# Performance work log

Hardware: AMD Instinct MI355X
Metric: run time of the kernel (lower is better)

Reference implementation:

```python
import jax, jax.numpy as jnp
import numpy as np

B, T, N, C, D = 8, 12, 1024, 64, 10

def setup_inputs() -> dict:
    key = jax.random.key(0)
    ks = jax.random.split(key, 7)
    x = jax.random.normal(ks[0], (B, T, N, C), dtype=jnp.float32)
    e1 = jax.random.normal(ks[1], (N, D), dtype=jnp.float32)
    e2 = jax.random.normal(ks[2], (N, D), dtype=jnp.float32)
    # buffer: sym-normalized adjacency after the __init__-time softmax
    A_sym = jax.random.uniform(ks[3], (N, N), dtype=jnp.float32)
    weights_pool = jax.random.normal(ks[4], (N, C, C), dtype=jnp.float32) * 0.02
    bias_pool = jax.random.normal(ks[5], (N, C), dtype=jnp.float32) * 0.02
    alpha = jnp.array([0.9], dtype=jnp.float32)
    beta = jnp.array([0.9], dtype=jnp.float32)
    gamma = jnp.array([0.1], dtype=jnp.float32)
    return {"x": x, "node_embeddings1": e1, "node_embeddings2": e2,
            "A_sym": A_sym, "weights_pool": weights_pool, "bias_pool": bias_pool,
            "alpha": alpha, "beta": beta, "gamma": gamma}


def reference(x, node_embeddings1, node_embeddings2, A_sym, weights_pool,
              bias_pool, alpha, beta, gamma):
    n = node_embeddings1.shape[0]
    # dynamic supports: relu(tanh(E1 E2^T - E2 E1^T)) + I
    s = jnp.tanh(node_embeddings1 @ node_embeddings2.T
                 - node_embeddings2 @ node_embeddings1.T)
    supports = jnp.eye(n, dtype=x.dtype) + jax.nn.relu(s)          # (N,N)

    # static branch: row-softmax of the precomputed sym-norm adjacency
    A = jax.nn.softmax(A_sym, axis=-1)                              # (N,N)
    x_static = jax.nn.relu(jnp.einsum('nm,btmc->btnc', A, x))       # (B,T,N,C)

    # spatial attention branch (note: softmax over the TIME axis, as in source)
    score = jnp.einsum('btnc,btmc->btnm', x, x)                     # (B,T,N,N)
    score = jax.nn.softmax(score, axis=1)
    x_sa = jax.nn.relu(jnp.einsum('btnm,btmc->btnc', score, x))     # (B,T,N,C)

    # adaptive graph conv: per-node weights/bias from supports
    weights = jnp.einsum('nd,dio->nio', supports, weights_pool)     # (N,C,C)
    bias = supports @ bias_pool                                     # (N,C)
    x_g = jnp.einsum('nm,btmc->btnc', supports, x)                  # (B,T,N,C)
    x_gconv = jax.nn.relu(jnp.einsum('btni,nio->btno', x_g, weights) + bias)

    return alpha * x_gconv + beta * x_sa + gamma * x_static
```

## Files before the change

### kernel.cpp

```cpp
#include <hip/hip_runtime.h>
#include <math.h>

#define Bdim 8
#define Tdim 12
#define BT   96
#define Ndim 1024
#define Cdim 64
#define Ddim 10
#define Jdim 6144
#define IOdim 4096

typedef __attribute__((ext_vector_type(4))) float f32x4;
typedef __attribute__((ext_vector_type(8))) short bf16x8;
typedef __attribute__((ext_vector_type(4))) _Float16 f16x4;

__device__ inline short f2bf(float f) {
    union { float f; unsigned u; } v; v.f = f;
    return (short)((v.u + 0x8000u) >> 16);
}
__device__ inline float bf2f(short s) {
    union { float f; unsigned u; } v; v.u = ((unsigned)(unsigned short)s) << 16;
    return v.f;
}
__device__ inline void load_lds16(const void* g, void* l) {
    __builtin_amdgcn_global_load_lds(
        (const __attribute__((address_space(1))) unsigned int*)g,
        (__attribute__((address_space(3))) unsigned int*)l, 16, 0, 0);
}
__device__ inline float fexp(float x) { return __expf(x); }
__device__ inline float frcp(float x) { return __builtin_amdgcn_rcpf(x); }
__device__ inline float flog(float x) { return __logf(x); }

__global__ __launch_bounds__(256) void k_supports(
    const float* __restrict__ e1, const float* __restrict__ e2,
    short* __restrict__ Sbf)
{
    int idx = blockIdx.x * 256 + threadIdx.x;
    int i = idx >> 10, j = idx & 1023;
    float s = 0.f;
#pragma unroll
    for (int d = 0; d < Ddim; ++d)
        s += e1[i * Ddim + d] * e2[j * Ddim + d]
           - e2[i * Ddim + d] * e1[j * Ddim + d];
    float t = 1.f - 2.f * frcp(fexp(2.f * s) + 1.f);
    float v = fmaxf(t, 0.f);
    if (i == j) v += 1.f;
    Sbf[idx] = f2bf(v);
}

__global__ __launch_bounds__(256) void k_softmax_rows(
    const float* __restrict__ In, short* __restrict__ Out)
{
    int row = blockIdx.x;
    const float* r = In + (size_t)row * Ndim;
    short* o = Out + (size_t)row * Ndim;
    __shared__ float red[256];
    int tid = threadIdx.x;
    float vals[4];
    float lmax = -INFINITY;
#pragma unroll
    for (int i = 0; i < 4; ++i) { vals[i] = r[tid + 256 * i]; lmax = fmaxf(lmax, vals[i]); }
    red[tid] = lmax; __syncthreads();
    for (int s = 128; s > 0; s >>= 1) {
        if (tid < s) red[tid] = fmaxf(red[tid], red[tid + s]);
        __syncthreads();
    }
    float m = red[0]; __syncthreads();
    float lsum = 0.f;
#pragma unroll
    for (int i = 0; i < 4; ++i) { vals[i] = fexp(vals[i] - m); lsum += vals[i]; }
    red[tid] = lsum; __syncthreads();
    for (int s = 128; s > 0; s >>= 1) {
        if (tid < s) red[tid] += red[tid + s];
        __syncthreads();
    }
    float inv = frcp(red[0]);
#pragma unroll
    for (int i = 0; i < 4; ++i) o[tid + 256 * i] = f2bf(vals[i] * inv);
}

__global__ __launch_bounds__(256) void k_cvt_x(
    const float* __restrict__ x, short* __restrict__ xbf, short* __restrict__ xT)
{
    __shared__ float Lt[64][65];
    int bt = blockIdx.y, n0 = blockIdx.x * 64;
    const float* src = x + (size_t)bt * 65536 + (size_t)n0 * 64;
    int tid = threadIdx.x;
#pragma unroll
    for (int p = 0; p < 4; ++p) {
        int idx = p * 256 + tid;
        int r = idx >> 4, c4 = idx & 15;
        float4 v = *(const float4*)&src[r * 64 + c4 * 4];
        short4 s4 = make_short4(f2bf(v.x), f2bf(v.y), f2bf(v.z), f2bf(v.w));
        *(short4*)&xbf[(size_t)bt * 65536 + (size_t)(n0 + r) * 64 + c4 * 4] = s4;
        Lt[r][c4 * 4 + 0] = v.x; Lt[r][c4 * 4 + 1] = v.y;
        Lt[r][c4 * 4 + 2] = v.z; Lt[r][c4 * 4 + 3] = v.w;
    }
    __syncthreads();
#pragma unroll
    for (int p = 0; p < 4; ++p) {
        int idx = p * 256 + tid;
        int c = idx >> 4, k4 = idx & 15;
        short4 s4 = make_short4(f2bf(Lt[k4 * 4 + 0][c]), f2bf(Lt[k4 * 4 + 1][c]),
                                f2bf(Lt[k4 * 4 + 2][c]), f2bf(Lt[k4 * 4 + 3][c]));
        *(short4*)&xT[(size_t)bt * 65536 + (size_t)c * 1024 + n0 + k4 * 4] = s4;
    }
}

__global__ __launch_bounds__(256) void k_cvt_wp(
    const float* __restrict__ wp, short* __restrict__ wpT)
{
    __shared__ float Lt[64][65];
    int k0 = blockIdx.y * 64, j0 = blockIdx.x * 64;
    int tid = threadIdx.x;
#pragma unroll
    for (int p = 0; p < 4; ++p) {
        int idx = p * 256 + tid;
        int r = idx >> 4, c4 = idx & 15;
        float4 v = *(const float4*)&wp[(size_t)(k0 + r) * IOdim + j0 + c4 * 4];
        Lt[r][c4 * 4 + 0] = v.x; Lt[r][c4 * 4 + 1] = v.y;
        Lt[r][c4 * 4 + 2] = v.z; Lt[r][c4 * 4 + 3] = v.w;
    }
    __syncthreads();
#pragma unroll
    for (int p = 0; p < 4; ++p) {
        int idx = p * 256 + tid;
        int c = idx >> 4, k4 = idx & 15;
        short4 s4 = make_short4(f2bf(Lt[k4 * 4 + 0][c]), f2bf(Lt[k4 * 4 + 1][c]),
                                f2bf(Lt[k4 * 4 + 2][c]), f2bf(Lt[k4 * 4 + 3][c]));
        *(short4*)&wpT[(size_t)(j0 + c) * 1024 + k0 + k4 * 4] = s4;
    }
}

__global__ __launch_bounds__(256) void k_cvt_bp(
    const float* __restrict__ bp, short* __restrict__ bpT)
{
    __shared__ float Lt[64][65];
    int k0 = blockIdx.x * 64;
    int tid = threadIdx.x;
#pragma unroll
    for (int p = 0; p < 4; ++p) {
        int idx = p * 256 + tid;
        int r = idx >> 4, c4 = idx & 15;
        float4 v = *(const float4*)&bp[(size_t)(k0 + r) * 64 + c4 * 4];
        Lt[r][c4 * 4 + 0] = v.x; Lt[r][c4 * 4 + 1] = v.y;
        Lt[r][c4 * 4 + 2] = v.z; Lt[r][c4 * 4 + 3] = v.w;
    }
    __syncthreads();
#pragma unroll
    for (int p = 0; p < 4; ++p) {
        int idx = p * 256 + tid;
        int c = idx >> 4, k4 = idx & 15;
        short4 s4 = make_short4(f2bf(Lt[k4 * 4 + 0][c]), f2bf(Lt[k4 * 4 + 1][c]),
                                f2bf(Lt[k4 * 4 + 2][c]), f2bf(Lt[k4 * 4 + 3][c]));
        *(short4*)&bpT[(size_t)c * 1024 + k0 + k4 * 4] = s4;
    }
}

template<int MODE>
__global__ __launch_bounds__(256) void k_gemm_bt(
    const short* __restrict__ A, const short* __restrict__ Bm,
    float* __restrict__ Cf, short* __restrict__ Cb,
    const float* __restrict__ gamma_p)
{
    __shared__ short At[128 * 64];
    __shared__ short Bt[128 * 64];
    const int tid = threadIdx.x;
    const int w = tid >> 6, l = tid & 63;
    const int l15 = l & 15, q = l >> 4;
    const int n0 = blockIdx.x * 128, j0 = blockIdx.y * 128;
    const int wr = (w & 1) * 64, wc = (w >> 1) * 64;
    const int lrow = l >> 3, lc8 = l & 7;

    f32x4 acc[4][4];
#pragma unroll
    for (int i = 0; i < 4; ++i)
#pragma unroll
        for (int j = 0; j < 4; ++j) acc[i][j] = (f32x4)0.f;

    for (int k0 = 0; k0 < 1024; k0 += 64) {
        __syncthreads();
#pragma unroll
        for (int p = 0; p < 4; ++p) {
            int r = p * 32 + w * 8 + lrow;
            int sc = lc8 ^ (r & 7);
            load_lds16(A + (size_t)(n0 + r) * 1024 + k0 + sc * 8,
                       &At[(p * 32 + w * 8) * 64]);
            load_lds16(Bm + (size_t)(j0 + r) * 1024 + k0 + sc * 8,
                       &Bt[(p * 32 + w * 8) * 64]);
        }
        __syncthreads();
#pragma unroll
        for (int ks = 0; ks < 2; ++ks) {
            bf16x8 af[4], bf[4];
#pragma unroll
            for (int rt = 0; rt < 4; ++rt) {
                int row = wr + rt * 16 + l15;
                int pos = (ks * 4 + q) ^ (row & 7);
                af[rt] = *(const bf16x8*)&At[row * 64 + pos * 8];
            }
#pragma unroll
            for (int ct = 0; ct < 4; ++ct) {
                int row = wc + ct * 16 + l15;
                int pos = (ks * 4 + q) ^ (row & 7);
                bf[ct] = *(const bf16x8*)&Bt[row * 64 + pos * 8];
            }
#pragma unroll
            for (int rt = 0; rt < 4; ++rt)
#pragma unroll
                for (int ct = 0; ct < 4; ++ct)
                    acc[rt][ct] = __builtin_amdgcn_mfma_f32_16x16x32_bf16(
                        af[rt], bf[ct], acc[rt][ct], 0, 0, 0);
        }
    }

    float gmm = (MODE == 0) ? gamma_p[0] : 0.f;
#pragma unroll
    for (int rt = 0; rt < 4; ++rt) {
        int nr = n0 + wr + rt * 16 + q * 4;
#pragma unroll
        for (int ct = 0; ct < 4; ++ct) {
            int j = j0 + wc + ct * 16 + l15;
#pragma unroll
            for (int r = 0; r < 4; ++r) {
                float v = acc[rt][ct][r];
                int n = nr + r;
                if (MODE == 1) {
                    Cb[(size_t)n * IOdim + j] = f2bf(v);
                } else if (n < 1024) {
                    int bt = j >> 6, c = j & 63;
                    Cf[(size_t)bt * 65536 + (size_t)n * 64 + c] = gmm * fmaxf(v, 0.f);
                } else {
                    Cb[(size_t)(n - 1024) * Jdim + j] = f2bf(v);
                }
            }
        }
    }
}

__global__ __launch_bounds__(256, 4) void k_sa_z(
    const short* __restrict__ xbf, short* __restrict__ Lh)
{
    __shared__ short Xn[64 * 64];
    __shared__ short Xm[64 * 64];

    int id = blockIdx.x;
    int b = id & 7;
    int r = id >> 3;
    int tn = 0, rr = r;
    while (rr >= 16 - tn) { rr -= 16 - tn; ++tn; }
    int tm = tn + rr;
    int tid = threadIdx.x;
    int w = tid >> 6, l = tid & 63;
    int l15 = l & 15, q = l >> 4;
    int lrow = l >> 3, lc8 = l & 7;
    int n0 = tn * 64, m0 = tm * 64;
    int wn = (w & 1) * 32, wm = (w >> 1) * 32;

    const short* Xb = xbf + (size_t)b * Tdim * Ndim * Cdim;
    short* Lb = Lh + ((size_t)b << 20);

    f32x4 M[2][2], Z[2][2];
#pragma unroll
    for (int nh = 0; nh < 2; ++nh)
#pragma unroll
        for (int mh = 0; mh < 2; ++mh) { M[nh][mh] = (f32x4)(-INFINITY); Z[nh][mh] = (f32x4)0.f; }

    for (int t = 0; t < Tdim; ++t) {
        const short* xt = Xb + (size_t)t * (Ndim * Cdim);
        __syncthreads();
#pragma unroll
        for (int p = 0; p < 2; ++p) {
            int rw = p * 32 + w * 8 + lrow;
            int sc = lc8 ^ (rw & 7);
            load_lds16(xt + (size_t)(n0 + rw) * 64 + sc * 8, &Xn[(p * 32 + w * 8) * 64]);
            load_lds16(xt + (size_t)(m0 + rw) * 64 + sc * 8, &Xm[(p * 32 + w * 8) * 64]);
        }
        __syncthreads();

        f32x4 sacc[2][2];
        sacc[0][0] = (f32x4)0.f; sacc[0][1] = (f32x4)0.f;
        sacc[1][0] = (f32x4)0.f; sacc[1][1] = (f32x4)0.f;
#pragma unroll
        for (int ch = 0; ch < 2; ++ch) {
            bf16x8 qb[2], af[2];
#pragma unroll
            for (int nh = 0; nh < 2; ++nh) {
                int row = wn + nh * 16 + l15;
                int pos = (ch * 4 + q) ^ (row & 7);
                qb[nh] = *(const bf16x8*)&Xn[row * 64 + pos * 8];
            }
#pragma unroll
            for (int mh = 0; mh < 2; ++mh) {
                int row = wm + mh * 16 + l15;
                int pos = (ch * 4 + q) ^ (row & 7);
                af[mh] = *(const bf16x8*)&Xm[row * 64 + pos * 8];
            }
#pragma unroll
            for (int nh = 0; nh < 2; ++nh)
#pragma unroll
                for (int mh = 0; mh < 2; ++mh)
                    sacc[nh][mh] = __builtin_amdgcn_mfma_f32_16x16x32_bf16(
                        af[mh], qb[nh], sacc[nh][mh], 0, 0, 0);
        }
#pragma unroll
        for (int nh = 0; nh < 2; ++nh)
#pragma unroll
            for (int mh = 0; mh < 2; ++mh)
#pragma unroll
                for (int i = 0; i < 4; ++i) {
                    float s  = sacc[nh][mh][i];
                    float mo = M[nh][mh][i];
                    float mn = fmaxf(mo, s);
                    Z[nh][mh][i] = Z[nh][mh][i] * fexp(mo - mn) + fexp(s - mn);
                    M[nh][mh][i] = mn;
                }
    }
#pragma unroll
    for (int nh = 0; nh < 2; ++nh)
#pragma unroll
        for (int mh = 0; mh < 2; ++mh) {
            f16x4 ev;
#pragma unroll
            for (int i = 0; i < 4; ++i)
                ev[i] = (_Float16)(M[nh][mh][i] + flog(Z[nh][mh][i]));
            int nn = n0 + wn + nh * 16 + l15;
            int mm = m0 + wm + mh * 16 + q * 4;
            *(f16x4*)&Lb[(size_t)nn * 1024 + mm] = ev;
            if (tn != tm) {
#pragma unroll
                for (int i = 0; i < 4; ++i)
                    Lb[(size_t)(mm + i) * 1024 + nn] = ((short*)&ev)[i];
            }
        }
}

__global__ __launch_bounds__(256, 3) void k_sa_pv(
    const short* __restrict__ xbf, const short* __restrict__ xT,
    const short* __restrict__ Lh, float* __restrict__ Out,
    const float* __restrict__ beta_p)
{
    __shared__ short Xm[2][64 * 64];
    __shared__ short XTl[2][64 * 64];
    __shared__ short Pl[4][16 * 64];

    int id = blockIdx.x;
    int b = id & 7;
    int r = id >> 3;
    int nt = r & 7, t = r >> 3;
    int tid = threadIdx.x;
    int w = tid >> 6, l = tid & 63;
    int l15 = l & 15, q = l >> 4;
    int n0 = nt * 128 + w * 32;

    const short* Xb  = xbf + ((size_t)b * Tdim + t) * (Ndim * Cdim);
    const short* XTb = xT  + ((size_t)b * Tdim + t) * (Ndim * Cdim);
    const short* Lb  = Lh + ((size_t)b << 20);

    int srow = tid >> 2, sc4 = tid & 3;

    bf16x8 qf[2][2];
#pragma unroll
    for (int nh = 0; nh < 2; ++nh)
#pragma unroll
        for (int ch = 0; ch < 2; ++ch)
            qf[nh][ch] = *(const bf16x8*)&Xb[(n0 + nh * 16 + l15) * 64 + ch * 32 + q * 8];

    f32x4 oacc[2][4];
#pragma unroll
    for (int nh = 0; nh < 2; ++nh)
#pragma unroll
        for (int ct = 0; ct < 4; ++ct) oacc[nh][ct] = (f32x4)0.f;

    bf16x8 v[2], v2[2];
#pragma unroll
    for (int p = 0; p < 2; ++p) {
        v[p]  = *(const bf16x8*)&Xb[(size_t)srow * 64 + (sc4 + 4 * p) * 8];
        v2[p] = *(const bf16x8*)&XTb[(size_t)srow * 1024 + (sc4 + 4 * p) * 8];
    }

    for (int mi = 0; mi < 16; ++mi) {
        int cur = mi & 1;
        int m0 = mi * 64;
#pragma unroll
        for (int p = 0; p < 2; ++p) {
            int g = sc4 + 4 * p;
            int pos = g ^ (srow & 7);
            *(bf16x8*)&Xm[cur][srow * 64 + pos * 8]  = v[p];
            *(bf16x8*)&XTl[cur][srow * 64 + pos * 8] = v2[p];
        }
        int m0n = (mi < 15) ? m0 + 64 : m0;
#pragma unroll
        for (int p = 0; p < 2; ++p) {
            v[p]  = *(const bf16x8*)&Xb[(size_t)(m0n + srow) * 64 + (sc4 + 4 * p) * 8];
            v2[p] = *(const bf16x8*)&XTb[(size_t)srow * 1024 + m0n + (sc4 + 4 * p) * 8];
        }
        f16x4 e[2][4];
#pragma unroll
        for (int nh = 0; nh < 2; ++nh)
#pragma unroll
            for (int mh = 0; mh < 4; ++mh)
                e[nh][mh] = *(const f16x4*)&Lb[(size_t)(n0 + nh * 16 + l15) * 1024
                                               + m0 + mh * 16 + q * 4];
        __syncthreads();

        f32x4 sacc[2][4];
#pragma unroll
        for (int nh = 0; nh < 2; ++nh)
#pragma unroll
            for (int mh = 0; mh < 4; ++mh) sacc[nh][mh] = (f32x4)0.f;
#pragma unroll
        for (int ch = 0; ch < 2; ++ch) {
#pragma unroll
            for (int mh = 0; mh < 4; ++mh) {
                int row = mh * 16 + l15;
                int pos = (ch * 4 + q) ^ (row & 7);
                bf16x8 af = *(const bf16x8*)&Xm[cur][row * 64 + pos * 8];
                sacc[0][mh] = __builtin_amdgcn_mfma_f32_16x16x32_bf16(
                    af, qf[0][ch], sacc[0][mh], 0, 0, 0);
                sacc[1][mh] = __builtin_amdgcn_mfma_f32_16x16x32_bf16(
                    af, qf[1][ch], sacc[1][mh], 0, 0, 0);
            }
        }
#pragma unroll
        for (int nh = 0; nh < 2; ++nh) {
#pragma unroll
            for (int mh = 0; mh < 4; ++mh) {
                f32x4 p = sacc[nh][mh];
                f16x4 ee = e[nh][mh];
                unsigned u0 = (unsigned)(unsigned short)f2bf(fexp(p[0] - (float)ee[0]))
                            | ((unsigned)(unsigned short)f2bf(fexp(p[1] - (float)ee[1])) << 16);
                unsigned u1 = (unsigned)(unsigned short)f2bf(fexp(p[2] - (float)ee[2]))
                            | ((unsigned)(unsigned short)f2bf(fexp(p[3] - (float)ee[3])) << 16);
                int g = mh * 2 + (q >> 1);
                int pos = g ^ (l15 & 7);
                *(uint2*)&Pl[w][l15 * 64 + pos * 8 + (q & 1) * 4] = make_uint2(u0, u1);
            }
#pragma unroll
            for (int ks = 0; ks < 2; ++ks) {
                int gr = ks * 4 + q;
                int pos = gr ^ (l15 & 7);
                bf16x8 pf = *(const bf16x8*)&Pl[w][l15 * 64 + pos * 8];
#pragma unroll
                for (int ct = 0; ct < 4; ++ct) {
                    int row = ct * 16 + l15;
                    int bp = (ks * 4 + q) ^ (row & 7);
                    bf16x8 bfr = *(const bf16x8*)&XTl[cur][row * 64 + bp * 8];
                    oacc[nh][ct] = __builtin_amdgcn_mfma_f32_16x16x32_bf16(
                        pf, bfr, oacc[nh][ct], 0, 0, 0);
                }
            }
        }
    }

    float beta = beta_p[0];
#pragma unroll
    for (int nh = 0; nh < 2; ++nh)
#pragma unroll
        for (int ct = 0; ct < 4; ++ct)
#pragma unroll
            for (int r2 = 0; r2 < 4; ++r2) {
                size_t idx = (((size_t)b * Tdim + t) * Ndim + n0 + nh * 16 + q * 4 + r2) * Cdim
                           + ct * 16 + l15;
                Out[idx] += beta * fmaxf(oacc[nh][ct][r2], 0.f);
            }
}

__global__ __launch_bounds__(256) void k_bias(
    const short* __restrict__ Sbf, const short* __restrict__ bpT,
    float* __restrict__ bias)
{
    int tid = threadIdx.x;
    int w = tid >> 6, l = tid & 63;
    int l15 = l & 15, q = l >> 4;
    int nr = blockIdx.x * 64 + w * 16;

    f32x4 acc[4];
#pragma unroll
    for (int ct = 0; ct < 4; ++ct) acc[ct] = (f32x4)0.f;

    for (int k0 = 0; k0 < 1024; k0 += 32) {
        bf16x8 af = *(const bf16x8*)&Sbf[(size_t)(nr + l15) * 1024 + k0 + q * 8];
#pragma unroll
        for (int ct = 0; ct < 4; ++ct) {
            bf16x8 bf = *(const bf16x8*)&bpT[(size_t)(ct * 16 + l15) * 1024 + k0 + q * 8];
            acc[ct] = __builtin_amdgcn_mfma_f32_16x16x32_bf16(af, bf, acc[ct], 0, 0, 0);
        }
    }
#pragma unroll
    for (int ct = 0; ct < 4; ++ct)
#pragma unroll
        for (int r = 0; r < 4; ++r)
            bias[(size_t)(nr + q * 4 + r) * 64 + ct * 16 + l15] = acc[ct][r];
}

__global__ __launch_bounds__(384) void k_gconv(
    const short* __restrict__ xgT, const short* __restrict__ Wb,
    const float* __restrict__ bias, float* __restrict__ Out,
    const float* __restrict__ alpha_p)
{
    __shared__ short Wl[64 * 64];
    int n = blockIdx.x;
    int tid = threadIdx.x;
    for (int f = tid; f < 512; f += 384) {
        int k = f >> 3, j = f & 7;
        *(bf16x8*)&Wl[k * 64 + (j ^ ((k >> 3) & 7)) * 8] =
            *(const bf16x8*)&Wb[(size_t)n * IOdim + f * 8];
    }
    __syncthreads();
    int w = tid / 64, l = tid & 63, l15 = l & 15, q = l >> 4;
    f32x4 acc[4];
#pragma unroll
    for (int ct = 0; ct < 4; ++ct) acc[ct] = (f32x4)0.f;
    const short* xr = xgT + (size_t)n * Jdim + (size_t)(w * 16 + l15) * 64;
#pragma unroll
    for (int ks = 0; ks < 2; ++ks) {
        bf16x8 a = *(const bf16x8*)&xr[ks * 32 + q * 8];
        int kb = ks * 32 + q * 8;
        int msk = (kb >> 3) & 7;
#pragma unroll
        for (int ct = 0; ct < 4; ++ct) {
            bf16x8 bfr;
#pragma unroll
            for (int e = 0; e < 8; ++e) {
                int o = ct * 16 + l15;
                bfr[e] = Wl[(kb + e) * 64 + (((o >> 3) ^ msk) * 8) + (o & 7)];
            }
            acc[ct] = __builtin_amdgcn_mfma_f32_16x16x32_bf16(a, bfr, acc[ct], 0, 0, 0);
        }
    }
    float alpha = alpha_p[0];
#pragma unroll
    for (int ct = 0; ct < 4; ++ct) {
        int o = ct * 16 + l15;
        float bo = bias[(size_t)n * 64 + o];
#pragma unroll
        for (int r = 0; r < 4; ++r) {
            int bt = w * 16 + q * 4 + r;
            size_t idx = (size_t)bt * 65536 + (size_t)n * 64 + o;
            Out[idx] += alpha * fmaxf(acc[ct][r] + bo, 0.f);
        }
    }
}

extern "C" void kernel_launch(void* const* d_in, const int* in_sizes, int n_in,
                              void* d_out, int out_size, void* d_ws, size_t ws_size,
                              hipStream_t stream)
{
    const float* x     = (const float*)d_in[0];
    const float* e1    = (const float*)d_in[1];
    const float* e2    = (const float*)d_in[2];
    const float* Asym  = (const float*)d_in[3];
    const float* wpool = (const float*)d_in[4];
    const float* bpool = (const float*)d_in[5];
    const float* alpha = (const float*)d_in[6];
    const float* beta  = (const float*)d_in[7];
    const float* gamma = (const float*)d_in[8];
    float* out = (float*)d_out;

    short* ASbf = (short*)d_ws;
    short* xbf  = ASbf + 2048 * 1024;
    short* xT   = xbf  + 6291456;
    short* wpT  = xT   + 6291456;
    short* Wbf  = wpT  + 4194304;
    short* xgT  = Wbf  + 4194304;
    float* bias = (float*)(xgT + 6291456);
    short* Lh   = (short*)(bias + 65536);
    short* bpT  = Lh + 8388608;

    k_supports<<<4096, 256, 0, stream>>>(e1, e2, ASbf + 1024 * 1024);
    k_softmax_rows<<<1024, 256, 0, stream>>>(Asym, ASbf);
    k_cvt_x<<<dim3(16, 96), 256, 0, stream>>>(x, xbf, xT);
    k_cvt_wp<<<dim3(64, 16), 256, 0, stream>>>(wpool, wpT);
    k_cvt_bp<<<16, 256, 0, stream>>>(bpool, bpT);
    k_sa_z<<<1088, 256, 0, stream>>>(xbf, Lh);
    k_gemm_bt<0><<<dim3(16, 48), 256, 0, stream>>>(ASbf, xT, out, xgT, gamma);
    k_gemm_bt<1><<<dim3(8, 32), 256, 0, stream>>>(ASbf + 1024 * 1024, wpT, nullptr, Wbf, nullptr);
    k_bias<<<16, 256, 0, stream>>>(ASbf + 1024 * 1024, bpT, bias);
    k_sa_pv<<<768, 256, 0, stream>>>(xbf, xT, Lh, out, beta);
    k_gconv<<<1024, 384, 0, stream>>>(xgT, Wbf, bias, out, alpha);
}
```

Before: 311.9 us.

## Merge prep kernels, swizzle GEMM block order, use exp2 and packed bf16 with setprio

Five preprocessing launches become two by dispatching on block index, which cuts per-launch overhead. The two GEMMs get a flat grid with an XCD-aware block remap meant to improve L2 locality. The log-sum-exp is now stored in base-2 so the attention PV kernel can use exp2 with one fma, and bf16 packing uses the v_cvt_pk_bf16_f32 instruction. s_setprio is placed around the MFMA sections. The packed conversion may round differently from the old manual f2bf routine, and the merged kernels carry unused LDS in some branches.

```diff
diff --git a/kernel.cpp b/kernel.cpp
--- a/kernel.cpp
+++ b/kernel.cpp
@@ -9,6 +9,7 @@
 #define Ddim 10
 #define Jdim 6144
 #define IOdim 4096
+#define LOG2E 1.44269504088896f
 
 typedef __attribute__((ext_vector_type(4))) float f32x4;
 typedef __attribute__((ext_vector_type(8))) short bf16x8;
@@ -29,131 +30,130 @@
 }
 __device__ inline float fexp(float x) { return __expf(x); }
 __device__ inline float frcp(float x) { return __builtin_amdgcn_rcpf(x); }
-__device__ inline float flog(float x) { return __logf(x); }
-
-__global__ __launch_bounds__(256) void k_supports(
+__device__ inline unsigned pk_bf16(float lo, float hi) {
+    unsigned r;
+    asm("v_cvt_pk_bf16_f32 %0, %1, %2" : "=v"(r) : "v"(lo), "v"(hi));
+    return r;
+}
+
+__global__ __launch_bounds__(256) void k_prep(
     const float* __restrict__ e1, const float* __restrict__ e2,
-    short* __restrict__ Sbf)
-{
-    int idx = blockIdx.x * 256 + threadIdx.x;
-    int i = idx >> 10, j = idx & 1023;
-    float s = 0.f;
-#pragma unroll
-    for (int d = 0; d < Ddim; ++d)
-        s += e1[i * Ddim + d] * e2[j * Ddim + d]
-           - e2[i * Ddim + d] * e1[j * Ddim + d];
-    float t = 1.f - 2.f * frcp(fexp(2.f * s) + 1.f);
-    float v = fmaxf(t, 0.f);
-    if (i == j) v += 1.f;
-    Sbf[idx] = f2bf(v);
-}
-
-__global__ __launch_bounds__(256) void k_softmax_rows(
-    const float* __restrict__ In, short* __restrict__ Out)
-{
-    int row = blockIdx.x;
-    const float* r = In + (size_t)row * Ndim;
-    short* o = Out + (size_t)row * Ndim;
+    short* __restrict__ Sup,
+    const float* __restrict__ Asym, short* __restrict__ SMout,
+    const float* __restrict__ bp, short* __restrict__ bpT)
+{
     __shared__ float red[256];
+    __shared__ float Lt[64][65];
+    int blk = blockIdx.x;
     int tid = threadIdx.x;
-    float vals[4];
-    float lmax = -INFINITY;
-#pragma unroll
-    for (int i = 0; i < 4; ++i) { vals[i] = r[tid + 256 * i]; lmax = fmaxf(lmax, vals[i]); }
-    red[tid] = lmax; __syncthreads();
-    for (int s = 128; s > 0; s >>= 1) {
-        if (tid < s) red[tid] = fmaxf(red[tid], red[tid + s]);
-        __syncthreads();
-    }
-    float m = red[0]; __syncthreads();
-    float lsum = 0.f;
-#pragma unroll
-    for (int i = 0; i < 4; ++i) { vals[i] = fexp(vals[i] - m); lsum += vals[i]; }
-    red[tid] = lsum; __syncthreads();
-    for (int s = 128; s > 0; s >>= 1) {
-        if (tid < s) red[tid] += red[tid + s];
-        __syncthreads();
-    }
-    float inv = frcp(red[0]);
-#pragma unroll
-    for (int i = 0; i < 4; ++i) o[tid + 256 * i] = f2bf(vals[i] * inv);
-}
-
-__global__ __launch_bounds__(256) void k_cvt_x(
-    const float* __restrict__ x, short* __restrict__ xbf, short* __restrict__ xT)
+    if (blk < 4096) {
+        int idx = blk * 256 + tid;
+        int i = idx >> 10, j = idx & 1023;
+        float s = 0.f;
+#pragma unroll
+        for (int d = 0; d < Ddim; ++d)
+            s += e1[i * Ddim + d] * e2[j * Ddim + d]
+               - e2[i * Ddim + d] * e1[j * Ddim + d];
+        float t = 1.f - 2.f * frcp(fexp(2.f * s) + 1.f);
+        float v = fmaxf(t, 0.f);
+        if (i == j) v += 1.f;
+        Sup[idx] = f2bf(v);
+    } else if (blk < 5120) {
+        int row = blk - 4096;
+        const float* r = Asym + (size_t)row * Ndim;
+        short* o = SMout + (size_t)row * Ndim;
+        float vals[4];
+        float lmax = -INFINITY;
+#pragma unroll
+        for (int i = 0; i < 4; ++i) { vals[i] = r[tid + 256 * i]; lmax = fmaxf(lmax, vals[i]); }
+        red[tid] = lmax; __syncthreads();
+        for (int s = 128; s > 0; s >>= 1) {
+            if (tid < s) red[tid] = fmaxf(red[tid], red[tid + s]);
+            __syncthreads();
+        }
+        float m = red[0]; __syncthreads();
+        float lsum = 0.f;
+#pragma unroll
+        for (int i = 0; i < 4; ++i) { vals[i] = fexp(vals[i] - m); lsum += vals[i]; }
+        red[tid] = lsum; __syncthreads();
+        for (int s = 128; s > 0; s >>= 1) {
+            if (tid < s) red[tid] += red[tid + s];
+            __syncthreads();
+        }
+        float inv = frcp(red[0]);
+#pragma unroll
+        for (int i = 0; i < 4; ++i) o[tid + 256 * i] = f2bf(vals[i] * inv);
+    } else {
+        int k0 = (blk - 5120) * 64;
+#pragma unroll
+        for (int p = 0; p < 4; ++p) {
+            int idx = p * 256 + tid;
+            int r = idx >> 4, c4 = idx & 15;
+            float4 v = *(const float4*)&bp[(size_t)(k0 + r) * 64 + c4 * 4];
+            Lt[r][c4 * 4 + 0] = v.x; Lt[r][c4 * 4 + 1] = v.y;
+            Lt[r][c4 * 4 + 2] = v.z; Lt[r][c4 * 4 + 3] = v.w;
+        }
+        __syncthreads();
+#pragma unroll
+        for (int p = 0; p < 4; ++p) {
+            int idx = p * 256 + tid;
+            int c = idx >> 4, k4 = idx & 15;
+            short4 s4 = make_short4(f2bf(Lt[k4 * 4 + 0][c]), f2bf(Lt[k4 * 4 + 1][c]),
+                                    f2bf(Lt[k4 * 4 + 2][c]), f2bf(Lt[k4 * 4 + 3][c]));
+            *(short4*)&bpT[(size_t)c * 1024 + k0 + k4 * 4] = s4;
+        }
+    }
+}
+
+__global__ __launch_bounds__(256) void k_cvt2(
+    const float* __restrict__ x, short* __restrict__ xbf, short* __restrict__ xT,
+    const float* __restrict__ wp, short* __restrict__ wpT)
 {
     __shared__ float Lt[64][65];
-    int bt = blockIdx.y, n0 = blockIdx.x * 64;
-    const float* src = x + (size_t)bt * 65536 + (size_t)n0 * 64;
+    int blk = blockIdx.x;
     int tid = threadIdx.x;
-#pragma unroll
-    for (int p = 0; p < 4; ++p) {
-        int idx = p * 256 + tid;
-        int r = idx >> 4, c4 = idx & 15;
-        float4 v = *(const float4*)&src[r * 64 + c4 * 4];
-        short4 s4 = make_short4(f2bf(v.x), f2bf(v.y), f2bf(v.z), f2bf(v.w));
-        *(short4*)&xbf[(size_t)bt * 65536 + (size_t)(n0 + r) * 64 + c4 * 4] = s4;
-        Lt[r][c4 * 4 + 0] = v.x; Lt[r][c4 * 4 + 1] = v.y;
-        Lt[r][c4 * 4 + 2] = v.z; Lt[r][c4 * 4 + 3] = v.w;
-    }
-    __syncthreads();
-#pragma unroll
-    for (int p = 0; p < 4; ++p) {
-        int idx = p * 256 + tid;
-        int c = idx >> 4, k4 = idx & 15;
-        short4 s4 = make_short4(f2bf(Lt[k4 * 4 + 0][c]), f2bf(Lt[k4 * 4 + 1][c]),
-                                f2bf(Lt[k4 * 4 + 2][c]), f2bf(Lt[k4 * 4 + 3][c]));
-        *(short4*)&xT[(size_t)bt * 65536 + (size_t)c * 1024 + n0 + k4 * 4] = s4;
-    }
-}
-
-__global__ __launch_bounds__(256) void k_cvt_wp(
-    const float* __restrict__ wp, short* __restrict__ wpT)
-{
-    __shared__ float Lt[64][65];
-    int k0 = blockIdx.y * 64, j0 = blockIdx.x * 64;
-    int tid = threadIdx.x;
-#pragma unroll
-    for (int p = 0; p < 4; ++p) {
-        int idx = p * 256 + tid;
-        int r = idx >> 4, c4 = idx & 15;
-        float4 v = *(const float4*)&wp[(size_t)(k0 + r) * IOdim + j0 + c4 * 4];
-        Lt[r][c4 * 4 + 0] = v.x; Lt[r][c4 * 4 + 1] = v.y;
-        Lt[r][c4 * 4 + 2] = v.z; Lt[r][c4 * 4 + 3] = v.w;
-    }
-    __syncthreads();
-#pragma unroll
-    for (int p = 0; p < 4; ++p) {
-        int idx = p * 256 + tid;
-        int c = idx >> 4, k4 = idx & 15;
-        short4 s4 = make_short4(f2bf(Lt[k4 * 4 + 0][c]), f2bf(Lt[k4 * 4 + 1][c]),
-                                f2bf(Lt[k4 * 4 + 2][c]), f2bf(Lt[k4 * 4 + 3][c]));
-        *(short4*)&wpT[(size_t)(j0 + c) * 1024 + k0 + k4 * 4] = s4;
-    }
-}
-
-__global__ __launch_bounds__(256) void k_cvt_bp(
-    const float* __restrict__ bp, short* __restrict__ bpT)
-{
-    __shared__ float Lt[64][65];
-    int k0 = blockIdx.x * 64;
-    int tid = threadIdx.x;
-#pragma unroll
-    for (int p = 0; p < 4; ++p) {
-        int idx = p * 256 + tid;
-        int r = idx >> 4, c4 = idx & 15;
-        float4 v = *(const float4*)&bp[(size_t)(k0 + r) * 64 + c4 * 4];
-        Lt[r][c4 * 4 + 0] = v.x; Lt[r][c4 * 4 + 1] = v.y;
-        Lt[r][c4 * 4 + 2] = v.z; Lt[r][c4 * 4 + 3] = v.w;
-    }
-    __syncthreads();
-#pragma unroll
-    for (int p = 0; p < 4; ++p) {
-        int idx = p * 256 + tid;
-        int c = idx >> 4, k4 = idx & 15;
-        short4 s4 = make_short4(f2bf(Lt[k4 * 4 + 0][c]), f2bf(Lt[k4 * 4 + 1][c]),
-                                f2bf(Lt[k4 * 4 + 2][c]), f2bf(Lt[k4 * 4 + 3][c]));
-        *(short4*)&bpT[(size_t)c * 1024 + k0 + k4 * 4] = s4;
+    if (blk < 1536) {
+        int bt = blk >> 4, n0 = (blk & 15) * 64;
+        const float* src = x + (size_t)bt * 65536 + (size_t)n0 * 64;
+#pragma unroll
+        for (int p = 0; p < 4; ++p) {
+            int idx = p * 256 + tid;
+            int r = idx >> 4, c4 = idx & 15;
+            float4 v = *(const float4*)&src[r * 64 + c4 * 4];
+            short4 s4 = make_short4(f2bf(v.x), f2bf(v.y), f2bf(v.z), f2bf(v.w));
+            *(short4*)&xbf[(size_t)bt * 65536 + (size_t)(n0 + r) * 64 + c4 * 4] = s4;
+            Lt[r][c4 * 4 + 0] = v.x; Lt[r][c4 * 4 + 1] = v.y;
+            Lt[r][c4 * 4 + 2] = v.z; Lt[r][c4 * 4 + 3] = v.w;
+        }
+        __syncthreads();
+#pragma unroll
+        for (int p = 0; p < 4; ++p) {
+            int idx = p * 256 + tid;
+            int c = idx >> 4, k4 = idx & 15;
+            short4 s4 = make_short4(f2bf(Lt[k4 * 4 + 0][c]), f2bf(Lt[k4 * 4 + 1][c]),
+                                    f2bf(Lt[k4 * 4 + 2][c]), f2bf(Lt[k4 * 4 + 3][c]));
+            *(short4*)&xT[(size_t)bt * 65536 + (size_t)c * 1024 + n0 + k4 * 4] = s4;
+        }
+    } else {
+        int b2 = blk - 1536;
+        int k0 = (b2 >> 6) * 64, j0 = (b2 & 63) * 64;
+#pragma unroll
+        for (int p = 0; p < 4; ++p) {
+            int idx = p * 256 + tid;
+            int r = idx >> 4, c4 = idx & 15;
+            float4 v = *(const float4*)&wp[(size_t)(k0 + r) * IOdim + j0 + c4 * 4];
+            Lt[r][c4 * 4 + 0] = v.x; Lt[r][c4 * 4 + 1] = v.y;
+            Lt[r][c4 * 4 + 2] = v.z; Lt[r][c4 * 4 + 3] = v.w;
+        }
+        __syncthreads();
+#pragma unroll
+        for (int p = 0; p < 4; ++p) {
+            int idx = p * 256 + tid;
+            int c = idx >> 4, k4 = idx & 15;
+            short4 s4 = make_short4(f2bf(Lt[k4 * 4 + 0][c]), f2bf(Lt[k4 * 4 + 1][c]),
+                                    f2bf(Lt[k4 * 4 + 2][c]), f2bf(Lt[k4 * 4 + 3][c]));
+            *(short4*)&wpT[(size_t)(j0 + c) * 1024 + k0 + k4 * 4] = s4;
+        }
     }
 }
 
@@ -168,7 +168,11 @@
     const int tid = threadIdx.x;
     const int w = tid >> 6, l = tid & 63;
     const int l15 = l & 15, q = l >> 4;
-    const int n0 = blockIdx.x * 128, j0 = blockIdx.y * 128;
+    const int nwg  = (MODE == 0) ? 768 : 256;
+    const int nbx  = (MODE == 0) ? 16 : 8;
+    int raw = blockIdx.x;
+    int sw  = (raw & 7) * (nwg >> 3) + (raw >> 3);
+    const int n0 = (sw % nbx) * 128, j0 = (sw / nbx) * 128;
     const int wr = (w & 1) * 64, wc = (w >> 1) * 64;
     const int lrow = l >> 3, lc8 = l & 7;
 
@@ -323,7 +327,7 @@
             f16x4 ev;
 #pragma unroll
             for (int i = 0; i < 4; ++i)
-                ev[i] = (_Float16)(M[nh][mh][i] + flog(Z[nh][mh][i]));
+                ev[i] = (_Float16)fmaf(M[nh][mh][i], LOG2E, __log2f(Z[nh][mh][i]));
             int nn = n0 + wn + nh * 16 + l15;
             int mm = m0 + wm + mh * 16 + q * 4;
             *(f16x4*)&Lb[(size_t)nn * 1024 + mm] = ev;
@@ -409,6 +413,7 @@
         for (int nh = 0; nh < 2; ++nh)
 #pragma unroll
             for (int mh = 0; mh < 4; ++mh) sacc[nh][mh] = (f32x4)0.f;
+        __builtin_amdgcn_s_setprio(1);
 #pragma unroll
         for (int ch = 0; ch < 2; ++ch) {
 #pragma unroll
@@ -422,20 +427,24 @@
                     af, qf[1][ch], sacc[1][mh], 0, 0, 0);
             }
         }
+        __builtin_amdgcn_s_setprio(0);
 #pragma unroll
         for (int nh = 0; nh < 2; ++nh) {
 #pragma unroll
             for (int mh = 0; mh < 4; ++mh) {
                 f32x4 p = sacc[nh][mh];
                 f16x4 ee = e[nh][mh];
-                unsigned u0 = (unsigned)(unsigned short)f2bf(fexp(p[0] - (float)ee[0]))
-                            | ((unsigned)(unsigned short)f2bf(fexp(p[1] - (float)ee[1])) << 16);
-                unsigned u1 = (unsigned)(unsigned short)f2bf(fexp(p[2] - (float)ee[2]))
-                            | ((unsigned)(unsigned short)f2bf(fexp(p[3] - (float)ee[3])) << 16);
+                float x0 = exp2f(fmaf(p[0], LOG2E, -(float)ee[0]));
+                float x1 = exp2f(fmaf(p[1], LOG2E, -(float)ee[1]));
+                float x2 = exp2f(fmaf(p[2], LOG2E, -(float)ee[2]));
+                float x3 = exp2f(fmaf(p[3], LOG2E, -(float)ee[3]));
+                unsigned u0 = pk_bf16(x0, x1);
+                unsigned u1 = pk_bf16(x2, x3);
                 int g = mh * 2 + (q >> 1);
                 int pos = g ^ (l15 & 7);
                 *(uint2*)&Pl[w][l15 * 64 + pos * 8 + (q & 1) * 4] = make_uint2(u0, u1);
             }
+            __builtin_amdgcn_s_setprio(1);
 #pragma unroll
             for (int ks = 0; ks < 2; ++ks) {
                 int gr = ks * 4 + q;
@@ -450,6 +459,7 @@
                         pf, bfr, oacc[nh][ct], 0, 0, 0);
                 }
             }
+            __builtin_amdgcn_s_setprio(0);
         }
     }
 
@@ -568,14 +578,11 @@
     short* Lh   = (short*)(bias + 65536);
     short* bpT  = Lh + 8388608;
 
-    k_supports<<<4096, 256, 0, stream>>>(e1, e2, ASbf + 1024 * 1024);
-    k_softmax_rows<<<1024, 256, 0, stream>>>(Asym, ASbf);
-    k_cvt_x<<<dim3(16, 96), 256, 0, stream>>>(x, xbf, xT);
-    k_cvt_wp<<<dim3(64, 16), 256, 0, stream>>>(wpool, wpT);
-    k_cvt_bp<<<16, 256, 0, stream>>>(bpool, bpT);
+    k_prep<<<5136, 256, 0, stream>>>(e1, e2, ASbf + 1024 * 1024, Asym, ASbf, bpool, bpT);
+    k_cvt2<<<2560, 256, 0, stream>>>(x, xbf, xT, wpool, wpT);
     k_sa_z<<<1088, 256, 0, stream>>>(xbf, Lh);
-    k_gemm_bt<0><<<dim3(16, 48), 256, 0, stream>>>(ASbf, xT, out, xgT, gamma);
-    k_gemm_bt<1><<<dim3(8, 32), 256, 0, stream>>>(ASbf + 1024 * 1024, wpT, nullptr, Wbf, nullptr);
+    k_gemm_bt<0><<<768, 256, 0, stream>>>(ASbf, xT, out, xgT, gamma);
+    k_gemm_bt<1><<<256, 256, 0, stream>>>(ASbf + 1024 * 1024, wpT, nullptr, Wbf, nullptr);
     k_bias<<<16, 256, 0, stream>>>(ASbf + 1024 * 1024, bpT, bias);
     k_sa_pv<<<768, 256, 0, stream>>>(xbf, xT, Lh, out, beta);
     k_gconv<<<1024, 384, 0, stream>>>(xgT, Wbf, bias, out, alpha);
```

After: 303.9 us. -2.6%, faster.
